# Kernel tuning notes

Measured on AMD Instinct MI355X. Metric: run time of the kernel, lower is better.

## Reference

```python
import jax, jax.numpy as jnp
import numpy as np
from jax import lax

KERNEL_SIZE = 11
SIGMA = 1.5
K1 = 0.01
K2 = 0.03
DATA_RANGE = 1.0


def _gaussian_kernel(size, sigma):
    coords = np.arange(size, dtype=np.float32) - (size - 1) / 2.0
    g = np.exp(-(coords[None, :] ** 2 + coords[:, None] ** 2) / (2.0 * sigma ** 2))
    g = g / g.sum()
    return jnp.asarray(g, dtype=jnp.float32)  # [k, k]


def _dwconv(x, k2d):
    # depthwise valid conv, groups = C (matches F.conv2d(..., groups=C))
    C = x.shape[1]
    w = jnp.broadcast_to(k2d[None, None], (C, 1, k2d.shape[0], k2d.shape[1]))
    return lax.conv_general_dilated(
        x, w, window_strides=(1, 1), padding='VALID',
        dimension_numbers=('NCHW', 'OIHW', 'NCHW'), feature_group_count=C)


def _avg_pool(x, f):
    # torch F.avg_pool2d(x, kernel_size=f) : stride=f, floor mode
    s = lax.reduce_window(x, 0.0, lax.add, (1, 1, f, f), (1, 1, f, f), 'VALID')
    return s / float(f * f)


def setup_inputs() -> dict:
    key = jax.random.key(0)
    kx, ky = jax.random.split(key)
    x = jax.random.uniform(kx, (32, 3, 512, 512), dtype=jnp.float32)
    y = jax.random.uniform(ky, (32, 3, 512, 512), dtype=jnp.float32)
    return {"x": x, "y": y}


def reference(x, y):
    x = x / DATA_RANGE
    y = y / DATA_RANGE
    # average-pool to roughly 256 resolution before SSIM (downsample=True)
    f = max(1, int(round(min(x.shape[-2], x.shape[-1]) / 256.0)))
    if f > 1:
        x = _avg_pool(x, f)
        y = _avg_pool(y, f)
    kern = _gaussian_kernel(KERNEL_SIZE, SIGMA)
    c1 = K1 ** 2
    c2 = K2 ** 2
    mu_x = _dwconv(x, kern)
    mu_y = _dwconv(y, kern)
    mu_xx = mu_x * mu_x
    mu_yy = mu_y * mu_y
    mu_xy = mu_x * mu_y
    sigma_xx = _dwconv(x * x, kern) - mu_xx
    sigma_yy = _dwconv(y * y, kern) - mu_yy
    sigma_xy = _dwconv(x * y, kern) - mu_xy
    cs = (2.0 * sigma_xy + c2) / (sigma_xx + sigma_yy + c2)
    ss = (2.0 * mu_xy + c1) / (mu_xx + mu_yy + c1) * cs
    ssim_val = ss.mean(axis=(-1, -2))          # [B, C]
    ssim_val = ssim_val.mean(axis=1)           # [B] mean over channels
    score = ssim_val.mean(axis=0)              # reduction='mean' over batch
    return 1.0 - score
```

## Files before the change

kernel.cpp:

```cpp
#include <hip/hip_runtime.h>


#define KS 11
#define H 8
#define ROWS (H + KS - 1)
#define NSTRIP 31
#define NPLANE 96
#define NWAVE (NPLANE * NSTRIP)
#define NBLOCK (NWAVE / 4)
#define OUTD 246
#define BUFW 272
#define C1V 1e-4f
#define C2V 9e-4f

__device__ __forceinline__ void load_pool(const float* __restrict__ xp,
                                          const float* __restrict__ yp,
                                          int r0, int i, int lane,
                                          float (&px)[4], float (&py)[4]) {
    int pr = r0 + i; pr = pr > 255 ? 255 : pr;
    const float* xr = xp + (size_t)(2 * pr) * 512 + 8 * lane;
    const float* yr = yp + (size_t)(2 * pr) * 512 + 8 * lane;
    float4 a0 = *(const float4*)xr;
    float4 a1 = *(const float4*)(xr + 4);
    float4 b0 = *(const float4*)(xr + 512);
    float4 b1 = *(const float4*)(xr + 516);
    float4 c0 = *(const float4*)yr;
    float4 c1 = *(const float4*)(yr + 4);
    float4 d0 = *(const float4*)(yr + 512);
    float4 d1 = *(const float4*)(yr + 516);
    px[0] = (a0.x + a0.y + b0.x + b0.y) * 0.25f;
    px[1] = (a0.z + a0.w + b0.z + b0.w) * 0.25f;
    px[2] = (a1.x + a1.y + b1.x + b1.y) * 0.25f;
    px[3] = (a1.z + a1.w + b1.z + b1.w) * 0.25f;
    py[0] = (c0.x + c0.y + d0.x + d0.y) * 0.25f;
    py[1] = (c0.z + c0.w + d0.z + d0.w) * 0.25f;
    py[2] = (c1.x + c1.y + d1.x + d1.y) * 0.25f;
    py[3] = (c1.z + c1.w + d1.z + d1.w) * 0.25f;
}

__device__ __forceinline__ void step_row(float* vb, const float (&wt)[KS],
                                         float (&rx)[KS][4], float (&ry)[KS][4],
                                         const float (&px)[4], const float (&py)[4],
                                         int lane, int ro, float& local) {
    #pragma unroll
    for (int c = 0; c < 4; ++c) { rx[KS - 1][c] = px[c]; ry[KS - 1][c] = py[c]; }

    float vmx[4] = {0,0,0,0}, vmy[4] = {0,0,0,0};
    float vxx[4] = {0,0,0,0}, vyy[4] = {0,0,0,0}, vxy[4] = {0,0,0,0};
    #pragma unroll
    for (int k = 0; k < KS; ++k) {
        float wk = wt[k];
        #pragma unroll
        for (int c = 0; c < 4; ++c) {
            float xv = rx[k][c], yv = ry[k][c];
            vmx[c] += wk * xv;       vmy[c] += wk * yv;
            vxx[c] += wk * xv * xv;  vyy[c] += wk * yv * yv;
            vxy[c] += wk * xv * yv;
        }
    }

    *(float4*)(vb + 0 * BUFW + 4 * lane) = make_float4(vmx[0], vmx[1], vmx[2], vmx[3]);
    *(float4*)(vb + 1 * BUFW + 4 * lane) = make_float4(vmy[0], vmy[1], vmy[2], vmy[3]);
    *(float4*)(vb + 2 * BUFW + 4 * lane) = make_float4(vxx[0], vxx[1], vxx[2], vxx[3]);
    *(float4*)(vb + 3 * BUFW + 4 * lane) = make_float4(vyy[0], vyy[1], vyy[2], vyy[3]);
    *(float4*)(vb + 4 * BUFW + 4 * lane) = make_float4(vxy[0], vxy[1], vxy[2], vxy[3]);
    __builtin_amdgcn_wave_barrier();

    float hp[5][4];
    #pragma unroll
    for (int p = 0; p < 5; ++p) {
        const float* bp = vb + p * BUFW + 4 * lane;
        float4 q0 = *(const float4*)bp;
        float4 q1 = *(const float4*)(bp + 4);
        float4 q2 = *(const float4*)(bp + 8);
        float4 q3 = *(const float4*)(bp + 12);
        float win[16] = {q0.x, q0.y, q0.z, q0.w, q1.x, q1.y, q1.z, q1.w,
                         q2.x, q2.y, q2.z, q2.w, q3.x, q3.y, q3.z, q3.w};
        #pragma unroll
        for (int c = 0; c < 4; ++c) {
            float a = 0.f;
            #pragma unroll
            for (int j = 0; j < KS; ++j) a += wt[j] * win[c + j];
            hp[p][c] = a;
        }
    }

    if (ro < OUTD) {
        #pragma unroll
        for (int c = 0; c < 4; ++c) {
            int oc = 4 * lane + c;
            float mx = hp[0][c], my = hp[1][c];
            float mxx = mx * mx, myy = my * my, mxy = mx * my;
            float sxx = hp[2][c] - mxx, syy = hp[3][c] - myy, sxy = hp[4][c] - mxy;
            float num = (2.f * mxy + C1V) * (2.f * sxy + C2V);
            float den = (mxx + myy + C1V) * (sxx + syy + C2V);
            float ss = num / den;
            local += (oc < OUTD) ? ss : 0.f;
        }
    }

    #pragma unroll
    for (int k = 0; k < KS - 1; ++k) {
        #pragma unroll
        for (int c = 0; c < 4; ++c) { rx[k][c] = rx[k + 1][c]; ry[k][c] = ry[k + 1][c]; }
    }
}

__global__ __launch_bounds__(256) void ssim_wave(const float* __restrict__ x,
                                                 const float* __restrict__ y,
                                                 double* __restrict__ partial) {
    __shared__ float vbuf[4][5][BUFW];
    const int tid = threadIdx.x;
    const int wv = tid >> 6, lane = tid & 63;
    const int gid = blockIdx.x * 4 + wv;
    const int plane = gid / NSTRIP, strip = gid % NSTRIP;
    const int r0 = strip * H;
    const float* xp = x + (size_t)plane * (512 * 512);
    const float* yp = y + (size_t)plane * (512 * 512);

    float wt[KS];
    {
        float s = 0.f;
        #pragma unroll
        for (int i = 0; i < KS; ++i) {
            float d = (float)i - 5.f;
            wt[i] = expf(-d * d / 4.5f);
            s += wt[i];
        }
        float inv = 1.f / s;
        #pragma unroll
        for (int i = 0; i < KS; ++i) wt[i] *= inv;
    }

    if (lane < BUFW - 256) {
        #pragma unroll
        for (int p = 0; p < 5; ++p)
            vbuf[wv][p][256 + lane] = 0.f;
    }
    __builtin_amdgcn_wave_barrier();

    float rx[KS][4], ry[KS][4];
    #pragma unroll
    for (int i = 0; i < KS - 1; ++i)
        load_pool(xp, yp, r0, i, lane, rx[i], ry[i]);

    float cpx[4], cpy[4], npx[4], npy[4];
    load_pool(xp, yp, r0, KS - 1, lane, cpx, cpy);
    float local = 0.f;
    float* vb = &vbuf[wv][0][0];

    #pragma unroll 1
    for (int i = KS - 1; i < ROWS; ++i) {
        load_pool(xp, yp, r0, i + 1, lane, npx, npy);
        step_row(vb, wt, rx, ry, cpx, cpy, lane, r0 + i - (KS - 1), local);
        #pragma unroll
        for (int c = 0; c < 4; ++c) { cpx[c] = npx[c]; cpy[c] = npy[c]; }
    }

    #pragma unroll
    for (int off = 32; off > 0; off >>= 1)
        local += __shfl_down(local, off, 64);
    if (lane == 0) partial[gid] = (double)local;
}

__global__ __launch_bounds__(256) void ssim_finalize(const double* __restrict__ partial,
                                                     float* __restrict__ out) {
    const int tid = threadIdx.x;
    double s = 0.0;
    for (int i = tid; i < NWAVE; i += 256) s += partial[i];
    #pragma unroll
    for (int off = 32; off > 0; off >>= 1)
        s += __shfl_down(s, off, 64);
    __shared__ double sd[4];
    if ((tid & 63) == 0) sd[tid >> 6] = s;
    __syncthreads();
    if (tid == 0) {
        double total = sd[0] + sd[1] + sd[2] + sd[3];
        const double n = (double)NPLANE * OUTD * OUTD;
        out[0] = (float)(1.0 - total / n);
    }
}

extern "C" void kernel_launch(void* const* d_in, const int* in_sizes, int n_in,
                              void* d_out, int out_size, void* d_ws, size_t ws_size,
                              hipStream_t stream) {
    const float* x = (const float*)d_in[0];
    const float* y = (const float*)d_in[1];
    float* out = (float*)d_out;
    double* partial = (double*)d_ws;

    ssim_wave<<<NBLOCK, 256, 0, stream>>>(x, y, partial);
    ssim_finalize<<<1, 256, 0, stream>>>(partial, out);
}
```

Before: 75.80 us.

## Enlarge row strips and defer pooling of prefetched rows past compute

Each wave now handles 12 output rows per strip instead of 8, which cuts the number of strips per plane from 31 to 21 and lowers the share of rows spent on the 10-row halo that must be reloaded. The next row's raw loads are issued before the row computation, and the 2x2 average pooling is done only after step_row, so the global loads can overlap the arithmetic. In exchange there are fewer waves in the grid, which can reduce occupancy and latency hiding, and keeping the 32 raw floats live adds register pressure.

```diff
diff --git a/kernel.cpp b/kernel.cpp
--- a/kernel.cpp
+++ b/kernel.cpp
@@ -2,9 +2,9 @@
 
 
 #define KS 11
-#define H 8
+#define H 12
 #define ROWS (H + KS - 1)
-#define NSTRIP 31
+#define NSTRIP 21
 #define NPLANE 96
 #define NWAVE (NPLANE * NSTRIP)
 #define NBLOCK (NWAVE / 4)
@@ -38,6 +38,35 @@
     py[3] = (c1.z + c1.w + d1.z + d1.w) * 0.25f;
 }
 
+__device__ __forceinline__ void issue_row(const float* __restrict__ xp,
+                                          const float* __restrict__ yp,
+                                          int r0, int i, int lane,
+                                          float4 (&rawx)[4], float4 (&rawy)[4]) {
+    int pr = r0 + i; pr = pr > 255 ? 255 : pr;
+    const float* xr = xp + (size_t)(2 * pr) * 512 + 8 * lane;
+    const float* yr = yp + (size_t)(2 * pr) * 512 + 8 * lane;
+    rawx[0] = *(const float4*)xr;
+    rawx[1] = *(const float4*)(xr + 4);
+    rawx[2] = *(const float4*)(xr + 512);
+    rawx[3] = *(const float4*)(xr + 516);
+    rawy[0] = *(const float4*)yr;
+    rawy[1] = *(const float4*)(yr + 4);
+    rawy[2] = *(const float4*)(yr + 512);
+    rawy[3] = *(const float4*)(yr + 516);
+}
+
+__device__ __forceinline__ void pool_raw(const float4 (&rawx)[4], const float4 (&rawy)[4],
+                                         float (&px)[4], float (&py)[4]) {
+    px[0] = (rawx[0].x + rawx[0].y + rawx[2].x + rawx[2].y) * 0.25f;
+    px[1] = (rawx[0].z + rawx[0].w + rawx[2].z + rawx[2].w) * 0.25f;
+    px[2] = (rawx[1].x + rawx[1].y + rawx[3].x + rawx[3].y) * 0.25f;
+    px[3] = (rawx[1].z + rawx[1].w + rawx[3].z + rawx[3].w) * 0.25f;
+    py[0] = (rawy[0].x + rawy[0].y + rawy[2].x + rawy[2].y) * 0.25f;
+    py[1] = (rawy[0].z + rawy[0].w + rawy[2].z + rawy[2].w) * 0.25f;
+    py[2] = (rawy[1].x + rawy[1].y + rawy[3].x + rawy[3].y) * 0.25f;
+    py[3] = (rawy[1].z + rawy[1].w + rawy[3].z + rawy[3].w) * 0.25f;
+}
+
 __device__ __forceinline__ void step_row(float* vb, const float (&wt)[KS],
                                          float (&rx)[KS][4], float (&ry)[KS][4],
                                          const float (&px)[4], const float (&py)[4],
@@ -144,17 +173,18 @@
     for (int i = 0; i < KS - 1; ++i)
         load_pool(xp, yp, r0, i, lane, rx[i], ry[i]);
 
-    float cpx[4], cpy[4], npx[4], npy[4];
+    float cpx[4], cpy[4];
     load_pool(xp, yp, r0, KS - 1, lane, cpx, cpy);
+
     float local = 0.f;
     float* vb = &vbuf[wv][0][0];
+    float4 rawx[4], rawy[4];
 
     #pragma unroll 1
     for (int i = KS - 1; i < ROWS; ++i) {
-        load_pool(xp, yp, r0, i + 1, lane, npx, npy);
+        issue_row(xp, yp, r0, i + 1, lane, rawx, rawy);
         step_row(vb, wt, rx, ry, cpx, cpy, lane, r0 + i - (KS - 1), local);
-        #pragma unroll
-        for (int c = 0; c < 4; ++c) { cpx[c] = npx[c]; cpy[c] = npy[c]; }
+        pool_raw(rawx, rawy, cpx, cpy);
     }
 
     #pragma unroll
```

Result: faster. 65.57 us (-13.5%).

## Taller strips and inline-asm prefetch of the next pooled row

Applied to the files above, without the earlier changes.

Raises the output rows per wave strip from 8 to 12, cutting the number of strips per plane from 31 to 21. This lowers the share of halo rows each wave reloads and recomputes. It also replaces the compiler-scheduled next-row load with hand-written global_load_dwordx4 inline assembly, issued a row ahead and waited on with an explicit s_waitcnt after the row compute, so the memory latency overlaps the convolution math. In exchange there are fewer waves to fill the GPU, and the compiler cannot see these hand-issued loads when it places its own vmcnt waits.

```diff
diff --git a/kernel.cpp b/kernel.cpp
--- a/kernel.cpp
+++ b/kernel.cpp
@@ -1,10 +1,12 @@
 #include <hip/hip_runtime.h>
 
 
+typedef float f32x4 __attribute__((ext_vector_type(4)));
+
 #define KS 11
-#define H 8
+#define H 12
 #define ROWS (H + KS - 1)
-#define NSTRIP 31
+#define NSTRIP 21
 #define NPLANE 96
 #define NWAVE (NPLANE * NSTRIP)
 #define NBLOCK (NWAVE / 4)
@@ -144,18 +146,54 @@
     for (int i = 0; i < KS - 1; ++i)
         load_pool(xp, yp, r0, i, lane, rx[i], ry[i]);
 
-    float cpx[4], cpy[4], npx[4], npy[4];
+    float cpx[4], cpy[4];
     load_pool(xp, yp, r0, KS - 1, lane, cpx, cpy);
+
     float local = 0.f;
     float* vb = &vbuf[wv][0][0];
 
+    f32x4 g0, g1, g2, g3, g4, g5, g6, g7;
+    #define ISSUE_ROW(I)                                                            \
+    {                                                                               \
+        int pr_ = r0 + (I); pr_ = pr_ > 255 ? 255 : pr_;                            \
+        const float* ax0_ = xp + (size_t)(2 * pr_) * 512 + 8 * lane;                \
+        const float* ax1_ = ax0_ + 512;                                             \
+        const float* ay0_ = yp + (size_t)(2 * pr_) * 512 + 8 * lane;                \
+        const float* ay1_ = ay0_ + 512;                                             \
+        asm volatile("global_load_dwordx4 %0, %1, off"           : "=v"(g0) : "v"(ax0_)); \
+        asm volatile("global_load_dwordx4 %0, %1, off offset:16" : "=v"(g1) : "v"(ax0_)); \
+        asm volatile("global_load_dwordx4 %0, %1, off"           : "=v"(g2) : "v"(ax1_)); \
+        asm volatile("global_load_dwordx4 %0, %1, off offset:16" : "=v"(g3) : "v"(ax1_)); \
+        asm volatile("global_load_dwordx4 %0, %1, off"           : "=v"(g4) : "v"(ay0_)); \
+        asm volatile("global_load_dwordx4 %0, %1, off offset:16" : "=v"(g5) : "v"(ay0_)); \
+        asm volatile("global_load_dwordx4 %0, %1, off"           : "=v"(g6) : "v"(ay1_)); \
+        asm volatile("global_load_dwordx4 %0, %1, off offset:16" : "=v"(g7) : "v"(ay1_)); \
+    }
+
+    ISSUE_ROW(KS);
+
     #pragma unroll 1
     for (int i = KS - 1; i < ROWS; ++i) {
-        load_pool(xp, yp, r0, i + 1, lane, npx, npy);
         step_row(vb, wt, rx, ry, cpx, cpy, lane, r0 + i - (KS - 1), local);
-        #pragma unroll
-        for (int c = 0; c < 4; ++c) { cpx[c] = npx[c]; cpy[c] = npy[c]; }
-    }
+
+        asm volatile("s_waitcnt vmcnt(0)"
+                     : "+v"(g0), "+v"(g1), "+v"(g2), "+v"(g3),
+                       "+v"(g4), "+v"(g5), "+v"(g6), "+v"(g7));
+
+        if (i < ROWS - 1) {
+            cpx[0] = (g0.x + g0.y + g2.x + g2.y) * 0.25f;
+            cpx[1] = (g0.z + g0.w + g2.z + g2.w) * 0.25f;
+            cpx[2] = (g1.x + g1.y + g3.x + g3.y) * 0.25f;
+            cpx[3] = (g1.z + g1.w + g3.z + g3.w) * 0.25f;
+            cpy[0] = (g4.x + g4.y + g6.x + g6.y) * 0.25f;
+            cpy[1] = (g4.z + g4.w + g6.z + g6.w) * 0.25f;
+            cpy[2] = (g5.x + g5.y + g7.x + g7.y) * 0.25f;
+            cpy[3] = (g5.z + g5.w + g7.z + g7.w) * 0.25f;
+        }
+        if (i < ROWS - 2) ISSUE_ROW(i + 2);
+    }
+
+    asm volatile("s_waitcnt vmcnt(0)");
 
     #pragma unroll
     for (int off = 32; off > 0; off >>= 1)
```

New measurement: 66.33 us. 12.5% less time.
